# Kernel optimization log

Measured on AMD Instinct MI355X. Metric: run time of the kernel, lower is better.

## Reference

```python
import jax, jax.numpy as jnp
import numpy as np

# Fano-plane triples defining octonion multiplication: e_a e_b = e_c (cyclic)
_TRIPLES = [(1, 2, 4), (2, 3, 5), (3, 4, 6), (4, 5, 7), (5, 6, 1), (6, 7, 2), (7, 1, 3)]


def _oct_structure():
    """S3[i,j,k] = sign s.t. e_i * e_j = s * e_k (zero otherwise)."""
    idx = np.zeros((8, 8), dtype=np.int32)
    sgn = np.zeros((8, 8), dtype=np.float32)
    for j in range(8):
        idx[0, j] = j; sgn[0, j] = 1.0
    for i in range(1, 8):
        idx[i, 0] = i; sgn[i, 0] = 1.0
        idx[i, i] = 0; sgn[i, i] = -1.0
    for a, b, c in _TRIPLES:
        for (p, q, r) in ((a, b, c), (b, c, a), (c, a, b)):
            idx[p, q] = r; sgn[p, q] = 1.0
            idx[q, p] = r; sgn[q, p] = -1.0
    S3 = np.zeros((8, 8, 8), dtype=np.float32)
    for i in range(8):
        for j in range(8):
            S3[i, j, idx[i, j]] = sgn[i, j]
    return jnp.asarray(S3)


def _oct_full(W, S3):
    """Fold octonion structure into a dense block matrix.

    W: [8, out8, in8] per-component weights. Effective map:
      y_k = sum_{i,j} S3[i,j,k] * W_i @ x_j  ->  M[k*out8:, j*in8:] = sum_i S3[i,j,k] W_i
    Returns [8*out8, 8*in8].
    """
    M = jnp.einsum('ijk,ion->kojn', S3, W)  # [8, out8, 8, in8]
    k8, o8, j8, n8 = M.shape
    return M.reshape(k8 * o8, j8 * n8)


def setup_inputs() -> dict:
    key = jax.random.key(0)
    ks = jax.random.split(key, 6)
    B, T, D = 8, 1024, 1024
    S = 2048  # d_state = n_embd * expand_factor
    x = jax.random.normal(ks[0], (B, T, D), dtype=jnp.float32)
    h_prev = jnp.zeros((B, S), dtype=jnp.float32)
    WA = jax.random.normal(ks[1], (8, S // 8, S // 8), dtype=jnp.float32) * float(1.0 / np.sqrt(S))
    WB = jax.random.normal(ks[2], (8, S // 8, D // 8), dtype=jnp.float32) * float(1.0 / np.sqrt(D))
    WC = jax.random.normal(ks[3], (8, D // 8, S // 8), dtype=jnp.float32) * float(1.0 / np.sqrt(S))
    Wdelta = jax.random.normal(ks[4], (S, D), dtype=jnp.float32) * float(1.0 / np.sqrt(D))
    delta_bias = jnp.full((S,), -2.0, dtype=jnp.float32)
    return dict(x=x, h_prev=h_prev, WA=WA, WB=WB, WC=WC, Wdelta=Wdelta, delta_bias=delta_bias)


def reference(x, h_prev, WA, WB, WC, Wdelta, delta_bias):
    S3 = _oct_structure()
    Af = _oct_full(WA, S3)  # [S, S]
    Bf = _oct_full(WB, S3)  # [S, D]
    Cf = _oct_full(WC, S3)  # [D, S]
    # Selective gate: sigmoid(x @ Wdelta^T + bias)  [B, T, S]
    delta = jax.nn.sigmoid(jnp.einsum('btd,sd->bts', x, Wdelta) + delta_bias)
    # Input injection precomputed for all timesteps (B is time-invariant)
    Bx = jnp.einsum('btd,sd->bts', x, Bf)  # [B, T, S]

    def step(h, inp):
        bx_t, d_t = inp  # [B, S], [B, S]
        h_new = (1.0 - d_t) * h + d_t * (h @ Af.T + bx_t)
        return h_new, h_new

    h_last, hs = jax.lax.scan(step, h_prev, (jnp.swapaxes(Bx, 0, 1), jnp.swapaxes(delta, 0, 1)))
    # Readout applied to the full state history at once: y[t] = C(h[t])
    y = jnp.einsum('tbs,ds->btd', hs, Cf)  # [B, T, D]
    return y, h_last
```

## Files before the change

### kernel.cpp

```cpp
#include <hip/hip_runtime.h>
#include <hip/hip_bf16.h>

#define T_STEPS 1024
#define OFF_AFT   0ull
#define OFF_GCAT  4194304ull
#define OFF_CFT   8388608ull
#define OFF_DELTA 10485760ull
#define OFF_BX    27262976ull
#define OFF_HS    44040192ull
#define OFF_HBUF  60817408ull

typedef short short8 __attribute__((ext_vector_type(8)));
typedef float f32x4 __attribute__((ext_vector_type(4)));

__device__ __forceinline__ void build_oct_tables(int tid, int (*Is)[8], float (*Sg)[8]) {
  if (tid < 64) {
    int i = tid >> 3, j = tid & 7;
    int k = 0; float s = 0.f;
    if (i == 0)      { k = j; s = 1.f; }
    else if (j == 0) { k = i; s = 1.f; }
    else if (i == j) { k = 0; s = -1.f; }
    else {
      const int T7[7][3] = {{1,2,4},{2,3,5},{3,4,6},{4,5,7},{5,6,1},{6,7,2},{7,1,3}};
      for (int t = 0; t < 7; ++t) {
        int a = T7[t][0], b = T7[t][1], c = T7[t][2];
        const int P[3][3] = {{a,b,c},{b,c,a},{c,a,b}};
        for (int r = 0; r < 3; ++r) {
          if (i == P[r][0] && j == P[r][1]) { k = P[r][2]; s = 1.f; }
          if (i == P[r][1] && j == P[r][0]) { k = P[r][2]; s = -1.f; }
        }
      }
    }
    Is[j][k] = i; Sg[j][k] = s;
  }
  __syncthreads();
}

__device__ __forceinline__ unsigned short bf16r(float x) {
  unsigned u = __float_as_uint(x);
  return (unsigned short)((u + 0x7FFFu + ((u >> 16) & 1u)) >> 16);
}

__global__ __launch_bounds__(256) void fold_Ab(const float* __restrict__ WA, unsigned short* __restrict__ AfB) {
  __shared__ int Is[8][8]; __shared__ float Sg[8][8];
  build_oct_tables(threadIdx.x, Is, Sg);
  int g8 = blockIdx.x * 256 + threadIdx.x;
  int sp = g8 >> 8;
  int s0 = (g8 & 255) * 8;
  int k8 = sp >> 8, o = sp & 255;
  int j8 = s0 >> 8, n = s0 & 255;
  int i = Is[j8][k8]; float sg = Sg[j8][k8];
  const float* src = WA + (size_t)i * 65536 + (size_t)o * 256 + n;
  float4 f0 = *(const float4*)(src);
  float4 f1 = *(const float4*)(src + 4);
  unsigned short v[8];
  v[0] = bf16r(sg * f0.x); v[1] = bf16r(sg * f0.y); v[2] = bf16r(sg * f0.z); v[3] = bf16r(sg * f0.w);
  v[4] = bf16r(sg * f1.x); v[5] = bf16r(sg * f1.y); v[6] = bf16r(sg * f1.z); v[7] = bf16r(sg * f1.w);
  *(short8*)(AfB + (size_t)g8 * 8) = *(short8*)v;
}

__global__ __launch_bounds__(256) void fold_GC(const float* __restrict__ Wd, const float* __restrict__ WB,
                                               float* __restrict__ Gcat) {
  __shared__ int Is[8][8]; __shared__ float Sg[8][8];
  build_oct_tables(threadIdx.x, Is, Sg);
  int g4 = blockIdx.x * 256 + threadIdx.x;
  int col = (g4 & 1023) * 4;
  int d = g4 >> 10;
  float4 v;
  if (col < 2048) {
    v.x = Wd[(size_t)(col + 0) * 1024 + d];
    v.y = Wd[(size_t)(col + 1) * 1024 + d];
    v.z = Wd[(size_t)(col + 2) * 1024 + d];
    v.w = Wd[(size_t)(col + 3) * 1024 + d];
  } else {
    int sp = col - 2048;
    int k = sp >> 8;
    int j = d >> 7, n = d & 127;
    int i = Is[j][k]; float sg = Sg[j][k];
    const float* wb = WB + (size_t)i * 32768 + n;
    v.x = sg * wb[(size_t)((sp + 0) & 255) * 128];
    v.y = sg * wb[(size_t)((sp + 1) & 255) * 128];
    v.z = sg * wb[(size_t)((sp + 2) & 255) * 128];
    v.w = sg * wb[(size_t)((sp + 3) & 255) * 128];
  }
  *(float4*)(Gcat + (size_t)g4 * 4) = v;
}

__global__ __launch_bounds__(256) void fold_C(const float* __restrict__ WC, float* __restrict__ CfT) {
  __shared__ int Is[8][8]; __shared__ float Sg[8][8];
  build_oct_tables(threadIdx.x, Is, Sg);
  int g4 = blockIdx.x * 256 + threadIdx.x;
  int d0 = (g4 & 255) * 4;
  int s  = g4 >> 8;
  int j = s >> 8, n = s & 255;
  int k = d0 >> 7;
  int i = Is[j][k]; float sg = Sg[j][k];
  const float* wc = WC + (size_t)i * 32768 + n;
  float4 v;
  v.x = sg * wc[(size_t)((d0 + 0) & 127) * 256];
  v.y = sg * wc[(size_t)((d0 + 1) & 127) * 256];
  v.z = sg * wc[(size_t)((d0 + 2) & 127) * 256];
  v.w = sg * wc[(size_t)((d0 + 3) & 127) * 256];
  *(float4*)(CfT + (size_t)g4 * 4) = v;
}

__global__ __launch_bounds__(256) void init_h(const float* __restrict__ h_prev, unsigned long long* __restrict__ hx) {
  int gid = blockIdx.x * 256 + threadIdx.x;
  if (gid < 8192) {
    int c = gid >> 6, within = gid & 63;
    int pr = within >> 3, b = within & 7;
    int s = c * 16 + pr * 2;
    unsigned pk = (unsigned)bf16r(h_prev[(size_t)b * 2048 + s])
                | ((unsigned)bf16r(h_prev[(size_t)b * 2048 + s + 1]) << 16);
    hx[gid] = ((unsigned long long)pk << 32) | 0ull;
  } else {
    hx[gid] = 0x00000000FFFFFFFFull;
  }
}

__global__ __launch_bounds__(256) void gemm_dbx(const float* __restrict__ X, const float* __restrict__ G,
                                                const float* __restrict__ bias,
                                                float* __restrict__ dlt, float* __restrict__ Bx) {
  __shared__ unsigned short Ah[128 * 40], Al[128 * 40];
  __shared__ unsigned short Bh[128 * 40], Bl[128 * 40];
  const int bn = blockIdx.x, bm = blockIdx.y;
  const int tid = threadIdx.x;
  const int lane = tid & 63;
  const int w = tid >> 6;
  const int wr = w >> 1, wc = w & 1;
  const int lr = lane & 15, lk = lane >> 4;

  f32x4 acc[4][4];
  #pragma unroll
  for (int a = 0; a < 4; ++a)
    #pragma unroll
    for (int b = 0; b < 4; ++b) acc[a][b] = (f32x4){0.f, 0.f, 0.f, 0.f};

  for (int kt = 0; kt < 1024; kt += 32) {
    {
      int row = tid >> 1, kh = tid & 1;
      const float* ar = X + (size_t)(bm * 128 + row) * 1024 + kt + kh * 16;
      float vv[16];
      #pragma unroll
      for (int q = 0; q < 4; ++q) {
        float4 f = *(const float4*)(ar + q * 4);
        vv[q * 4 + 0] = f.x; vv[q * 4 + 1] = f.y; vv[q * 4 + 2] = f.z; vv[q * 4 + 3] = f.w;
      }
      unsigned* ah32 = (unsigned*)Ah + row * 20 + kh * 8;
      unsigned* al32 = (unsigned*)Al + row * 20 + kh * 8;
      #pragma unroll
      for (int j = 0; j < 8; ++j) {
        unsigned short h0 = bf16r(vv[2 * j]), h1 = bf16r(vv[2 * j + 1]);
        float r0 = vv[2 * j]     - __uint_as_float((unsigned)h0 << 16);
        float r1 = vv[2 * j + 1] - __uint_as_float((unsigned)h1 << 16);
        unsigned short l0 = bf16r(r0), l1 = bf16r(r1);
        ah32[j] = (unsigned)h0 | ((unsigned)h1 << 16);
        al32[j] = (unsigned)l0 | ((unsigned)l1 << 16);
      }
    }
    {
      int kr = tid >> 3, cg = tid & 7;
      const float* br = G + (size_t)(kt + kr) * 4096 + bn * 128 + cg * 16;
      #pragma unroll
      for (int q = 0; q < 4; ++q) {
        float4 f = *(const float4*)(br + q * 4);
        float vv[4] = {f.x, f.y, f.z, f.w};
        #pragma unroll
        for (int e = 0; e < 4; ++e) {
          int n = cg * 16 + q * 4 + e;
          unsigned short h = bf16r(vv[e]);
          float r = vv[e] - __uint_as_float((unsigned)h << 16);
          Bh[n * 40 + kr] = h;
          Bl[n * 40 + kr] = bf16r(r);
        }
      }
    }
    __syncthreads();
    short8 ah[4], al[4], bh[4], bl[4];
    #pragma unroll
    for (int f = 0; f < 4; ++f) {
      int ma = (wr * 64 + f * 16 + lr) * 40 + lk * 8;
      int nb = (wc * 64 + f * 16 + lr) * 40 + lk * 8;
      ah[f] = *(const short8*)(Ah + ma);
      al[f] = *(const short8*)(Al + ma);
      bh[f] = *(const short8*)(Bh + nb);
      bl[f] = *(const short8*)(Bl + nb);
    }
    #pragma unroll
    for (int fm = 0; fm < 4; ++fm)
      #pragma unroll
      for (int fn = 0; fn < 4; ++fn) {
        acc[fm][fn] = __builtin_amdgcn_mfma_f32_16x16x32_bf16(ah[fm], bh[fn], acc[fm][fn], 0, 0, 0);
        acc[fm][fn] = __builtin_amdgcn_mfma_f32_16x16x32_bf16(ah[fm], bl[fn], acc[fm][fn], 0, 0, 0);
        acc[fm][fn] = __builtin_amdgcn_mfma_f32_16x16x32_bf16(al[fm], bh[fn], acc[fm][fn], 0, 0, 0);
      }
    __syncthreads();
  }
  const bool isDelta = (bn < 16);
  #pragma unroll
  for (int fm = 0; fm < 4; ++fm) {
    #pragma unroll
    for (int rr = 0; rr < 4; ++rr) {
      int r = bm * 128 + wr * 64 + fm * 16 + lk * 4 + rr;
      int t = r & 1023, b = r >> 10;
      size_t base = ((size_t)t * 8 + b) * 2048;
      #pragma unroll
      for (int fn = 0; fn < 4; ++fn) {
        int n = bn * 128 + wc * 64 + fn * 16 + lr;
        float v = acc[fm][fn][rr];
        if (isDelta) {
          v += bias[n];
          v = 1.0f / (1.0f + expf(-v));
          dlt[base + n] = v;
        } else {
          Bx[base + (n - 2048)] = v;
        }
      }
    }
  }
}

__global__ __launch_bounds__(256) void gemm_y(const float* __restrict__ HS, const float* __restrict__ CfT,
                                              float* __restrict__ out) {
  __shared__ unsigned short As[128 * 40];
  __shared__ unsigned short Bs[128 * 40];
  const int bn = blockIdx.x, bm = blockIdx.y;
  const int tid = threadIdx.x;
  const int lane = tid & 63;
  const int w = tid >> 6;
  const int wr = w >> 1, wc = w & 1;
  const int lr = lane & 15, lk = lane >> 4;

  f32x4 acc[4][4];
  #pragma unroll
  for (int a = 0; a < 4; ++a)
    #pragma unroll
    for (int b = 0; b < 4; ++b) acc[a][b] = (f32x4){0.f, 0.f, 0.f, 0.f};

  for (int kt = 0; kt < 2048; kt += 32) {
    {
      int row = tid >> 1, kh = tid & 1;
      int rg = bm * 128 + row;
      const float* ar = HS + (size_t)((rg & 1023) * 8 + (rg >> 10)) * 2048 + kt + kh * 16;
      float vv[16];
      #pragma unroll
      for (int q = 0; q < 4; ++q) {
        float4 f = *(const float4*)(ar + q * 4);
        vv[q * 4 + 0] = f.x; vv[q * 4 + 1] = f.y; vv[q * 4 + 2] = f.z; vv[q * 4 + 3] = f.w;
      }
      unsigned* a32 = (unsigned*)As + row * 20 + kh * 8;
      #pragma unroll
      for (int j = 0; j < 8; ++j)
        a32[j] = (unsigned)bf16r(vv[2 * j]) | ((unsigned)bf16r(vv[2 * j + 1]) << 16);
    }
    {
      int kr = tid >> 3, cg = tid & 7;
      const float* br = CfT + (size_t)(kt + kr) * 1024 + bn * 128 + cg * 16;
      #pragma unroll
      for (int q = 0; q < 4; ++q) {
        float4 f = *(const float4*)(br + q * 4);
        float vv[4] = {f.x, f.y, f.z, f.w};
        #pragma unroll
        for (int e = 0; e < 4; ++e)
          Bs[(cg * 16 + q * 4 + e) * 40 + kr] = bf16r(vv[e]);
      }
    }
    __syncthreads();
    short8 aF[4], bF[4];
    #pragma unroll
    for (int f = 0; f < 4; ++f) {
      aF[f] = *(const short8*)(As + (wr * 64 + f * 16 + lr) * 40 + lk * 8);
      bF[f] = *(const short8*)(Bs + (wc * 64 + f * 16 + lr) * 40 + lk * 8);
    }
    #pragma unroll
    for (int fm = 0; fm < 4; ++fm)
      #pragma unroll
      for (int fn = 0; fn < 4; ++fn)
        acc[fm][fn] = __builtin_amdgcn_mfma_f32_16x16x32_bf16(aF[fm], bF[fn], acc[fm][fn], 0, 0, 0);
    __syncthreads();
  }
  #pragma unroll
  for (int fm = 0; fm < 4; ++fm)
    #pragma unroll
    for (int rr = 0; rr < 4; ++rr) {
      size_t rg = bm * 128 + wr * 64 + fm * 16 + lk * 4 + rr;
      #pragma unroll
      for (int fn = 0; fn < 4; ++fn) {
        int n = bn * 128 + wc * 64 + fn * 16 + lr;
        out[rg * 1024 + n] = acc[fm][fn][rr];
      }
    }
}

__global__ __launch_bounds__(512) void scan_kernel(const unsigned short* __restrict__ AfB,
                                                   const float* __restrict__ dlt,
                                                   const float* __restrict__ Bx, float* __restrict__ hs,
                                                   unsigned long long* __restrict__ hx,
                                                   const float* __restrict__ h_prev, float* __restrict__ hlast) {
  __shared__ float red[8 * 144];
  const int wg = blockIdx.x;
  const int tid = threadIdx.x;
  const int lane = tid & 63;
  const int w = tid >> 6;
  const int row = lane & 15;
  const int g4 = lane >> 4;
  const int nb = lane & 7;

  short8 afr[8];
  {
    const unsigned short* ab = AfB + (size_t)(wg * 16 + row) * 2048 + w * 256 + g4 * 8;
    #pragma unroll
    for (int q = 0; q < 8; ++q)
      afr[q] = *(const short8*)(ab + q * 32);
  }
  const int ubase = w * 1024 + (g4 >> 1) * 64 + (g4 & 1) * 32 + nb;

  const int ub = tid >> 3, usp = (tid & 7) * 2;
  const int pword = wg * 64 + (tid & 7) * 8 + ub;
  float hr0 = 0.f, hr1 = 0.f;
  if (tid < 64) {
    hr0 = h_prev[(size_t)ub * 2048 + wg * 16 + usp];
    hr1 = h_prev[(size_t)ub * 2048 + wg * 16 + usp + 1];
  }

  #pragma unroll 1
  for (int t = 0; t < T_STEPS; ++t) {
    float2 dv = make_float2(0.f, 0.f), bxv = make_float2(0.f, 0.f);
    if (tid < 64) {
      size_t off = ((size_t)t * 8 + ub) * 2048 + wg * 16 + usp;
      dv  = *(const float2*)(dlt + off);
      bxv = *(const float2*)(Bx + off);
    }
    const unsigned want = (unsigned)t;
    const unsigned long long* bq = hx + (size_t)(t & 1) * 8192;
    unsigned long long wv[32];
    #pragma unroll
    for (int j = 0; j < 32; ++j)
      wv[j] = __hip_atomic_load(bq + ubase + (j >> 2) * 128 + (j & 3) * 8,
                                __ATOMIC_RELAXED, __HIP_MEMORY_SCOPE_SYSTEM);
    for (;;) {
      bool stale = false;
      #pragma unroll
      for (int j = 0; j < 32; ++j) stale |= ((unsigned)wv[j] != want);
      if (!__any(stale)) break;
      #pragma unroll
      for (int j = 0; j < 32; ++j)
        if ((unsigned)wv[j] != want)
          wv[j] = __hip_atomic_load(bq + ubase + (j >> 2) * 128 + (j & 3) * 8,
                                    __ATOMIC_RELAXED, __HIP_MEMORY_SCOPE_SYSTEM);
    }
    f32x4 acc = {0.f, 0.f, 0.f, 0.f};
    #pragma unroll
    for (int q = 0; q < 8; ++q) {
      union { unsigned d[4]; short8 v; } bb;
      bb.d[0] = (unsigned)(wv[q * 4 + 0] >> 32);
      bb.d[1] = (unsigned)(wv[q * 4 + 1] >> 32);
      bb.d[2] = (unsigned)(wv[q * 4 + 2] >> 32);
      bb.d[3] = (unsigned)(wv[q * 4 + 3] >> 32);
      acc = __builtin_amdgcn_mfma_f32_16x16x32_bf16(afr[q], bb.v, acc, 0, 0, 0);
    }
    if (row < 8) {
      #pragma unroll
      for (int r = 0; r < 4; ++r)
        red[w * 144 + (g4 * 4 + r) * 9 + row] = acc[r];
    }
    __syncthreads();
    if (tid < 64) {
      float o0 = 0.f, o1 = 0.f;
      #pragma unroll
      for (int ww = 0; ww < 8; ++ww) {
        o0 += red[ww * 144 + usp * 9 + ub];
        o1 += red[ww * 144 + (usp + 1) * 9 + ub];
      }
      float h0 = fmaf(dv.x, o0 + bxv.x - hr0, hr0);
      float h1 = fmaf(dv.y, o1 + bxv.y - hr1, hr1);
      hr0 = h0; hr1 = h1;
      size_t off = ((size_t)t * 8 + ub) * 2048 + wg * 16 + usp;
      *(float2*)(hs + off) = make_float2(h0, h1);
      unsigned pk = (unsigned)bf16r(h0) | ((unsigned)bf16r(h1) << 16);
      unsigned long long wval = ((unsigned long long)pk << 32) | (unsigned long long)(unsigned)(t + 1);
      __hip_atomic_store(hx + (size_t)((t + 1) & 1) * 8192 + pword, wval,
                         __ATOMIC_RELAXED, __HIP_MEMORY_SCOPE_SYSTEM);
      if (t == T_STEPS - 1)
        *(float2*)(hlast + (size_t)ub * 2048 + wg * 16 + usp) = make_float2(h0, h1);
    }
    __syncthreads();
  }
}

extern "C" void kernel_launch(void* const* d_in, const int* in_sizes, int n_in,
                              void* d_out, int out_size, void* d_ws, size_t ws_size,
                              hipStream_t stream) {
  const float* x      = (const float*)d_in[0];
  const float* h_prev = (const float*)d_in[1];
  const float* WA     = (const float*)d_in[2];
  const float* WB     = (const float*)d_in[3];
  const float* WC     = (const float*)d_in[4];
  const float* Wd     = (const float*)d_in[5];
  const float* bias   = (const float*)d_in[6];
  float* out = (float*)d_out;
  float* w = (float*)d_ws;
  unsigned short* AfB = (unsigned short*)(w + OFF_AFT);
  float* Gcat = w + OFF_GCAT;
  float* CfT  = w + OFF_CFT;
  float* dlt  = w + OFF_DELTA;
  float* Bx   = w + OFF_BX;
  float* hs   = w + OFF_HS;
  unsigned long long* hx = (unsigned long long*)(w + OFF_HBUF);

  fold_Ab<<<2048, 256, 0, stream>>>(WA, AfB);
  fold_GC<<<4096, 256, 0, stream>>>(Wd, WB, Gcat);
  fold_C <<<2048, 256, 0, stream>>>(WC, CfT);
  init_h <<<64,   256, 0, stream>>>(h_prev, hx);
  gemm_dbx<<<dim3(32, 64), 256, 0, stream>>>(x, Gcat, bias, dlt, Bx);
  scan_kernel<<<128, 512, 0, stream>>>(AfB, dlt, Bx, hs, hx, h_prev, out + 8388608);
  gemm_y<<<dim3(8, 64), 256, 0, stream>>>(hs, CfT, out);
}
```

Measured before the change: 4.326 ms.

## Split scan per batch row so each workgroup syncs only within its batch group

Repartitions the recurrent scan so that each of 256 workgroups owns 64 state rows for a single batch element, rather than 16 rows across all 8 batches. Each wave now issues four MFMAs per k-slice, one per 16-row tile, and polls only its own batch's 2048-entry flag buffer, so cross-workgroup dependencies are confined to 32 blocks instead of 128. Only one batch column of each MFMA output is used, which wastes most of the matrix throughput. A double-buffered reduction array also removes the second __syncthreads per step, at the cost of more register pressure from the four A-fragment sets.

Measured after the change: 5.721 ms. +32.2%, slower.

```diff
diff --git a/kernel.cpp b/kernel.cpp
--- a/kernel.cpp
+++ b/kernel.cpp
@@ -106,12 +106,11 @@
 
 __global__ __launch_bounds__(256) void init_h(const float* __restrict__ h_prev, unsigned long long* __restrict__ hx) {
   int gid = blockIdx.x * 256 + threadIdx.x;
-  if (gid < 8192) {
-    int c = gid >> 6, within = gid & 63;
-    int pr = within >> 3, b = within & 7;
-    int s = c * 16 + pr * 2;
-    unsigned pk = (unsigned)bf16r(h_prev[(size_t)b * 2048 + s])
-                | ((unsigned)bf16r(h_prev[(size_t)b * 2048 + s + 1]) << 16);
+  int g = gid >> 11, widx = gid & 2047;
+  if (widx < 1024) {
+    int s = widx * 2;
+    unsigned pk = (unsigned)bf16r(h_prev[(size_t)g * 2048 + s])
+                | ((unsigned)bf16r(h_prev[(size_t)g * 2048 + s + 1]) << 16);
     hx[gid] = ((unsigned long long)pk << 32) | 0ull;
   } else {
     hx[gid] = 0x00000000FFFFFFFFull;
@@ -153,9 +152,8 @@
         unsigned short h0 = bf16r(vv[2 * j]), h1 = bf16r(vv[2 * j + 1]);
         float r0 = vv[2 * j]     - __uint_as_float((unsigned)h0 << 16);
         float r1 = vv[2 * j + 1] - __uint_as_float((unsigned)h1 << 16);
-        unsigned short l0 = bf16r(r0), l1 = bf16r(r1);
         ah32[j] = (unsigned)h0 | ((unsigned)h1 << 16);
-        al32[j] = (unsigned)l0 | ((unsigned)l1 << 16);
+        al32[j] = (unsigned)bf16r(r0) | ((unsigned)bf16r(r1) << 16);
       }
     }
     {
@@ -297,59 +295,66 @@
                                                    const float* __restrict__ Bx, float* __restrict__ hs,
                                                    unsigned long long* __restrict__ hx,
                                                    const float* __restrict__ h_prev, float* __restrict__ hlast) {
-  __shared__ float red[8 * 144];
+  __shared__ float red[2][8 * 68];
   const int wg = blockIdx.x;
+  const int g = wg >> 5;
+  const int m = wg & 31;
   const int tid = threadIdx.x;
   const int lane = tid & 63;
   const int w = tid >> 6;
   const int row = lane & 15;
   const int g4 = lane >> 4;
-  const int nb = lane & 7;
-
-  short8 afr[8];
-  {
-    const unsigned short* ab = AfB + (size_t)(wg * 16 + row) * 2048 + w * 256 + g4 * 8;
+
+  short8 afr[4][8];
+  #pragma unroll
+  for (int mt = 0; mt < 4; ++mt) {
+    const unsigned short* ab = AfB + (size_t)(m * 64 + mt * 16 + row) * 2048 + w * 256 + g4 * 8;
     #pragma unroll
     for (int q = 0; q < 8; ++q)
-      afr[q] = *(const short8*)(ab + q * 32);
-  }
-  const int ubase = w * 1024 + (g4 >> 1) * 64 + (g4 & 1) * 32 + nb;
-
-  const int ub = tid >> 3, usp = (tid & 7) * 2;
-  const int pword = wg * 64 + (tid & 7) * 8 + ub;
+      afr[mt][q] = *(const short8*)(ab + q * 32);
+  }
+  unsigned long long* hxg = hx + (size_t)g * 2048;
+
   float hr0 = 0.f, hr1 = 0.f;
-  if (tid < 64) {
-    hr0 = h_prev[(size_t)ub * 2048 + wg * 16 + usp];
-    hr1 = h_prev[(size_t)ub * 2048 + wg * 16 + usp + 1];
+  if (tid < 32) {
+    hr0 = h_prev[(size_t)g * 2048 + m * 64 + tid * 2];
+    hr1 = h_prev[(size_t)g * 2048 + m * 64 + tid * 2 + 1];
   }
 
   #pragma unroll 1
   for (int t = 0; t < T_STEPS; ++t) {
     float2 dv = make_float2(0.f, 0.f), bxv = make_float2(0.f, 0.f);
-    if (tid < 64) {
-      size_t off = ((size_t)t * 8 + ub) * 2048 + wg * 16 + usp;
+    if (tid < 32) {
+      size_t off = ((size_t)t * 8 + g) * 2048 + m * 64 + tid * 2;
       dv  = *(const float2*)(dlt + off);
       bxv = *(const float2*)(Bx + off);
     }
     const unsigned want = (unsigned)t;
-    const unsigned long long* bq = hx + (size_t)(t & 1) * 8192;
+    const unsigned long long* bq = hxg + (size_t)(t & 1) * 1024;
+    const int wb = w * 128 + g4 * 4;
     unsigned long long wv[32];
     #pragma unroll
-    for (int j = 0; j < 32; ++j)
-      wv[j] = __hip_atomic_load(bq + ubase + (j >> 2) * 128 + (j & 3) * 8,
-                                __ATOMIC_RELAXED, __HIP_MEMORY_SCOPE_SYSTEM);
+    for (int q = 0; q < 8; ++q)
+      #pragma unroll
+      for (int u = 0; u < 4; ++u)
+        wv[q * 4 + u] = __hip_atomic_load(bq + wb + q * 16 + u,
+                                          __ATOMIC_RELAXED, __HIP_MEMORY_SCOPE_SYSTEM);
     for (;;) {
       bool stale = false;
       #pragma unroll
       for (int j = 0; j < 32; ++j) stale |= ((unsigned)wv[j] != want);
       if (!__any(stale)) break;
       #pragma unroll
-      for (int j = 0; j < 32; ++j)
-        if ((unsigned)wv[j] != want)
-          wv[j] = __hip_atomic_load(bq + ubase + (j >> 2) * 128 + (j & 3) * 8,
-                                    __ATOMIC_RELAXED, __HIP_MEMORY_SCOPE_SYSTEM);
-    }
-    f32x4 acc = {0.f, 0.f, 0.f, 0.f};
+      for (int q = 0; q < 8; ++q)
+        #pragma unroll
+        for (int u = 0; u < 4; ++u)
+          if ((unsigned)wv[q * 4 + u] != want)
+            wv[q * 4 + u] = __hip_atomic_load(bq + wb + q * 16 + u,
+                                              __ATOMIC_RELAXED, __HIP_MEMORY_SCOPE_SYSTEM);
+    }
+    f32x4 acc[4];
+    #pragma unroll
+    for (int mt = 0; mt < 4; ++mt) acc[mt] = (f32x4){0.f, 0.f, 0.f, 0.f};
     #pragma unroll
     for (int q = 0; q < 8; ++q) {
       union { unsigned d[4]; short8 v; } bb;
@@ -357,34 +362,36 @@
       bb.d[1] = (unsigned)(wv[q * 4 + 1] >> 32);
       bb.d[2] = (unsigned)(wv[q * 4 + 2] >> 32);
       bb.d[3] = (unsigned)(wv[q * 4 + 3] >> 32);
-      acc = __builtin_amdgcn_mfma_f32_16x16x32_bf16(afr[q], bb.v, acc, 0, 0, 0);
-    }
-    if (row < 8) {
-      #pragma unroll
-      for (int r = 0; r < 4; ++r)
-        red[w * 144 + (g4 * 4 + r) * 9 + row] = acc[r];
+      #pragma unroll
+      for (int mt = 0; mt < 4; ++mt)
+        acc[mt] = __builtin_amdgcn_mfma_f32_16x16x32_bf16(afr[mt][q], bb.v, acc[mt], 0, 0, 0);
+    }
+    float* rb = &red[t & 1][0];
+    if (row == 0) {
+      #pragma unroll
+      for (int mt = 0; mt < 4; ++mt)
+        *(f32x4*)(&rb[w * 68 + mt * 16 + g4 * 4]) = acc[mt];
     }
     __syncthreads();
-    if (tid < 64) {
+    if (tid < 32) {
       float o0 = 0.f, o1 = 0.f;
       #pragma unroll
       for (int ww = 0; ww < 8; ++ww) {
-        o0 += red[ww * 144 + usp * 9 + ub];
-        o1 += red[ww * 144 + (usp + 1) * 9 + ub];
+        o0 += rb[ww * 68 + tid * 2];
+        o1 += rb[ww * 68 + tid * 2 + 1];
       }
       float h0 = fmaf(dv.x, o0 + bxv.x - hr0, hr0);
       float h1 = fmaf(dv.y, o1 + bxv.y - hr1, hr1);
       hr0 = h0; hr1 = h1;
-      size_t off = ((size_t)t * 8 + ub) * 2048 + wg * 16 + usp;
-      *(float2*)(hs + off) = make_float2(h0, h1);
       unsigned pk = (unsigned)bf16r(h0) | ((unsigned)bf16r(h1) << 16);
       unsigned long long wval = ((unsigned long long)pk << 32) | (unsigned long long)(unsigned)(t + 1);
-      __hip_atomic_store(hx + (size_t)((t + 1) & 1) * 8192 + pword, wval,
+      __hip_atomic_store(hxg + (size_t)((t + 1) & 1) * 1024 + m * 32 + tid, wval,
                          __ATOMIC_RELAXED, __HIP_MEMORY_SCOPE_SYSTEM);
+      size_t off = ((size_t)t * 8 + g) * 2048 + m * 64 + tid * 2;
+      *(float2*)(hs + off) = make_float2(h0, h1);
       if (t == T_STEPS - 1)
-        *(float2*)(hlast + (size_t)ub * 2048 + wg * 16 + usp) = make_float2(h0, h1);
-    }
-    __syncthreads();
+        *(float2*)(hlast + (size_t)g * 2048 + m * 64 + tid * 2) = make_float2(h0, h1);
+    }
   }
 }
 
@@ -413,6 +420,6 @@
   fold_C <<<2048, 256, 0, stream>>>(WC, CfT);
   init_h <<<64,   256, 0, stream>>>(h_prev, hx);
   gemm_dbx<<<dim3(32, 64), 256, 0, stream>>>(x, Gcat, bias, dlt, Bx);
-  scan_kernel<<<128, 512, 0, stream>>>(AfB, dlt, Bx, hs, hx, h_prev, out + 8388608);
+  scan_kernel<<<256, 512, 0, stream>>>(AfB, dlt, Bx, hs, hx, h_prev, out + 8388608);
   gemm_y<<<dim3(8, 64), 256, 0, stream>>>(hs, CfT, out);
 }
```
